# Optimization experiments

Hardware: AMD Instinct MI355X
Metric: run time of the kernel (lower is better)

## Reference

```python
import jax, jax.numpy as jnp
import numpy as np


def setup_inputs() -> dict:
    key = jax.random.key(0)
    x = jax.random.normal(key, (32, 512, 56, 56), dtype=jnp.float32)
    return {"x": x}


def reference(x):
    n, c, h, w = x.shape
    f = x.reshape(n, c, h * w)                       # (n, c, hw)
    f_norm = jax.nn.softmax(f * 7.0, axis=2)         # softmax over spatial
    bilinear = jnp.einsum('ncs,nds->ncd', f_norm, f) # (n, c, c)
    bilinear = jax.nn.softmax(bilinear, axis=2)      # softmax over channel 'keys'
    trilinear = jnp.einsum('ncd,nds->ncs', bilinear, f).reshape(n, c, h, w)
    trilinear = jax.lax.stop_gradient(trilinear)     # matches torch .detach()
    structure_att = jnp.sum(trilinear, axis=1, keepdims=True)  # (n, 1, h, w)
    return structure_att
```

## Files before the change

### kernel.cpp

```cpp
#include <hip/hip_runtime.h>
#include <stdint.h>


#define NB 32
#define CC 512
#define SS 3136
#define SCALE 7.0f

typedef float f32x4 __attribute__((ext_vector_type(4)));
typedef _Float16 f16x8 __attribute__((ext_vector_type(8)));
typedef _Float16 f16x4 __attribute__((ext_vector_type(4)));
typedef _Float16 f16x2 __attribute__((ext_vector_type(2)));

__device__ inline unsigned short f2bf(float f) {
  unsigned int u = __float_as_uint(f);
  u += 0x7fffu + ((u >> 16) & 1u);
  return (unsigned short)(u >> 16);
}
__device__ inline float bf2f(unsigned short u) {
  return __uint_as_float((uint32_t)u << 16);
}

__device__ inline float wredmax(float v) {
#pragma unroll
  for (int m = 32; m >= 1; m >>= 1) v = fmaxf(v, __shfl_xor(v, m, 64));
  return v;
}
__device__ inline float wredsum(float v) {
#pragma unroll
  for (int m = 32; m >= 1; m >>= 1) v += __shfl_xor(v, m, 64);
  return v;
}

__device__ inline void load_lds16(const void* g, void* l) {
  __builtin_amdgcn_global_load_lds(
      (const __attribute__((address_space(1))) void*)(uintptr_t)g,
      (__attribute__((address_space(3))) void*)(uintptr_t)l, 16, 0, 0);
}

__global__ __launch_bounds__(256) void k_prep(const float* __restrict__ x,
                                              unsigned short* __restrict__ t,
                                              float* __restrict__ inv7,
                                              float* __restrict__ mxv,
                                              float* __restrict__ esum) {
  const int row = blockIdx.x;
  const int tid = threadIdx.x;
  if (tid == 0) esum[row] = 0.f;
  const float4* xr = (const float4*)(x + (size_t)row * SS);
  float4 v0 = xr[tid];
  float4 v1 = xr[tid + 256];
  float4 v2 = xr[tid + 512];
  float4 v3 = (tid < 16) ? xr[768 + tid] : make_float4(-1e30f, -1e30f, -1e30f, -1e30f);

  float mx = fmaxf(fmaxf(fmaxf(v0.x, v0.y), fmaxf(v0.z, v0.w)),
             fmaxf(fmaxf(fmaxf(v1.x, v1.y), fmaxf(v1.z, v1.w)),
             fmaxf(fmaxf(fmaxf(v2.x, v2.y), fmaxf(v2.z, v2.w)),
                   fmaxf(fmaxf(v3.x, v3.y), fmaxf(v3.z, v3.w)))));
  __shared__ float redm[4], reds[4];
  mx = wredmax(mx);
  if ((tid & 63) == 0) redm[tid >> 6] = mx;
  __syncthreads();
  mx = fmaxf(fmaxf(redm[0], redm[1]), fmaxf(redm[2], redm[3]));

  float s = 0.f;
  f16x4 p0, p1, p2, p3;
#define TQ(dst, sv)                                        \
  {                                                        \
    _Float16 th = (_Float16)(SCALE * ((sv) - mx));         \
    (dst) = th;                                            \
    s += (float)(_Float16)__expf((float)th);               \
  }
  TQ(p0[0], v0.x) TQ(p0[1], v0.y) TQ(p0[2], v0.z) TQ(p0[3], v0.w)
  TQ(p1[0], v1.x) TQ(p1[1], v1.y) TQ(p1[2], v1.z) TQ(p1[3], v1.w)
  TQ(p2[0], v2.x) TQ(p2[1], v2.y) TQ(p2[2], v2.z) TQ(p2[3], v2.w)
  TQ(p3[0], v3.x) TQ(p3[1], v3.y) TQ(p3[2], v3.z) TQ(p3[3], v3.w)
#undef TQ
  s = wredsum(s);
  if ((tid & 63) == 0) reds[tid >> 6] = s;
  __syncthreads();

  f16x4* tr = (f16x4*)(t + (size_t)row * SS);
  tr[tid] = p0;
  tr[tid + 256] = p1;
  tr[tid + 512] = p2;
  if (tid < 16) tr[768 + tid] = p3;
  if (tid == 0) {
    const float stot = reds[0] + reds[1] + reds[2] + reds[3];
    inv7[row] = 1.0f / (SCALE * stot);
    mxv[row] = mx;
  }
}

#define BM 128
#define BK 64

__global__ __launch_bounds__(256) void k_gemm(const unsigned short* __restrict__ T,
                                              unsigned short* __restrict__ P,
                                              const float* __restrict__ inv7,
                                              const float* __restrict__ mxv,
                                              float* __restrict__ esum) {
  __shared__ unsigned short sA[BM * BK];
  __shared__ unsigned short sB[BM * BK];
  const int lin  = blockIdx.y * gridDim.x + blockIdx.x;
  const int xcd  = lin & 7;
  const int slot = lin >> 3;
  const int pair = xcd * 16 + (slot >> 2);
  const int n    = pair >> 2;
  const int tm   = (pair & 3) * BM;
  const int tn   = (slot & 3) * BM;
  const unsigned short* Ap = T + (size_t)n * CC * SS + (size_t)tm * SS;
  const unsigned short* Bp = T + (size_t)n * CC * SS + (size_t)tn * SS;
  const int tid  = threadIdx.x;
  const int lane = tid & 63;
  const int wave = tid >> 6;
  const int wm   = (wave >> 1) * 64;
  const int wn   = (wave & 1) * 64;
  const int quad = lane >> 4;
  const int rr   = lane & 15;

  f32x4 acc[4][4] = {};

  for (int k0 = 0; k0 < SS; k0 += BK) {
    f16x8 hv[4];
#pragma unroll
    for (int tt = 0; tt < 4; tt++) {
      const int j  = ((tt << 2) + wave) * 64 + lane;
      const int r  = j >> 3;
      const int cg = (j & 7) ^ (r & 7);
      hv[tt] = *(const f16x8*)(Ap + (size_t)r * SS + (k0 + cg * 8));
      load_lds16(Bp + (size_t)r * SS + (k0 + cg * 8), &sB[(size_t)j * 8]);
    }
#pragma unroll
    for (int tt = 0; tt < 4; tt++) {
      const int j = ((tt << 2) + wave) * 64 + lane;
      f16x8 ev;
#pragma unroll
      for (int u = 0; u < 8; u++) ev[u] = (_Float16)__expf((float)hv[tt][u]);
      *(f16x8*)&sA[(size_t)j * 8] = ev;
    }
    __syncthreads();
#pragma unroll
    for (int ki = 0; ki < 2; ki++) {
      f16x8 af[4], bfr[4];
      const int cg = ki * 4 + quad;
#pragma unroll
      for (int mt = 0; mt < 4; mt++) {
        const int r  = wm + mt * 16 + rr;
        const int cs = cg ^ (r & 7);
        af[mt] = *(const f16x8*)&sA[(r * 8 + cs) * 8];
      }
#pragma unroll
      for (int nt = 0; nt < 4; nt++) {
        const int r  = wn + nt * 16 + rr;
        const int cs = cg ^ (r & 7);
        bfr[nt] = *(const f16x8*)&sB[(r * 8 + cs) * 8];
      }
#pragma unroll
      for (int mt = 0; mt < 4; mt++)
#pragma unroll
        for (int nt = 0; nt < 4; nt++)
          acc[mt][nt] = __builtin_amdgcn_mfma_f32_16x16x32_f16(af[mt], bfr[nt], acc[mt][nt], 0, 0, 0);
    }
    __syncthreads();
  }

  unsigned short* Pp = P + ((size_t)n << 18);
  float mxd[4];
#pragma unroll
  for (int nt = 0; nt < 4; nt++) mxd[nt] = mxv[n * CC + tn + wn + nt * 16 + rr];
#pragma unroll
  for (int mt = 0; mt < 4; mt++) {
    const int rbase = tm + wm + mt * 16 + quad * 4;
    float iv[4];
#pragma unroll
    for (int i = 0; i < 4; i++) iv[i] = inv7[n * CC + rbase + i];
    float rs[4] = {0.f, 0.f, 0.f, 0.f};
#pragma unroll
    for (int nt = 0; nt < 4; nt++) {
      const int col = tn + wn + nt * 16 + rr;
#pragma unroll
      for (int i = 0; i < 4; i++) {
        const float e = __expf(acc[mt][nt][i] * iv[i] + mxd[nt]);
        rs[i] += e;
        Pp[(size_t)(rbase + i) * CC + col] = f2bf(e);
      }
    }
#pragma unroll
    for (int i = 0; i < 4; i++) {
      float v = rs[i];
#pragma unroll
      for (int m = 8; m >= 1; m >>= 1) v += __shfl_xor(v, m, 64);
      if (rr == 0) atomicAdd(&esum[n * CC + rbase + i], v);
    }
  }
}

__global__ __launch_bounds__(256) void k_wsum(const unsigned short* __restrict__ P,
                                              const float* __restrict__ esum,
                                              float* __restrict__ wp,
                                              float* __restrict__ outz) {
  const int lin  = blockIdx.y * gridDim.x + blockIdx.x;
  const int xcd  = lin & 7;
  const int slot = lin >> 3;
  const int n    = xcd * 4 + (slot & 3);
  const int g    = (slot >> 2) & 7;
  const int d    = (slot >> 5) * 256 + threadIdx.x;
  __shared__ float sinv[64];
  if (threadIdx.x < 64) sinv[threadIdx.x] = 1.0f / esum[n * CC + g * 64 + threadIdx.x];
  __syncthreads();
  const unsigned short* p = P + (size_t)n * CC * CC + (size_t)(g * 64) * CC + d;
  float acc = 0.f;
#pragma unroll 8
  for (int c = 0; c < 64; c++) acc += bf2f(p[(size_t)c * CC]) * sinv[c];
  wp[((size_t)n * 8 + g) * CC + d] = acc;
  const int idx = lin * 256 + threadIdx.x;
  if (idx < NB * SS) outz[idx] = 0.f;
}

__global__ __launch_bounds__(256) void k_out(const unsigned short* __restrict__ T,
                                             const float* __restrict__ wp,
                                             const float* __restrict__ mxv,
                                             float* __restrict__ out) {
  const int n  = blockIdx.y >> 2;
  const int dq = blockIdx.y & 3;
  const int s0 = (blockIdx.x * 256 + threadIdx.x) * 2;
  __shared__ float sw[128];
  __shared__ float sc[2];
  if (threadIdx.x < 128) {
    float v = 0.f;
#pragma unroll
    for (int g = 0; g < 8; g++) v += wp[((size_t)n * 8 + g) * CC + dq * 128 + threadIdx.x];
    sw[threadIdx.x] = v * (1.0f / SCALE);
    float pm = v * mxv[n * CC + dq * 128 + threadIdx.x];
    pm = wredsum(pm);
    if ((threadIdx.x & 63) == 0) sc[threadIdx.x >> 6] = pm;
  }
  __syncthreads();
  const float csum = sc[0] + sc[1];
  if (s0 >= SS) return;
  const unsigned short* bp = T + (size_t)n * CC * SS + (size_t)(dq * 128) * SS + s0;
  float a0 = 0.f, a1 = 0.f;
#pragma unroll 8
  for (int d = 0; d < 128; d++) {
    const f16x2 hv = *(const f16x2*)(bp + (size_t)d * SS);
    a0 += sw[d] * (float)hv[0];
    a1 += sw[d] * (float)hv[1];
  }
  atomicAdd(&out[(size_t)n * SS + s0], a0 + csum);
  atomicAdd(&out[(size_t)n * SS + s0 + 1], a1 + csum);
}

extern "C" void kernel_launch(void* const* d_in, const int* in_sizes, int n_in,
                              void* d_out, int out_size, void* d_ws, size_t ws_size,
                              hipStream_t stream) {
  const float* x = (const float*)d_in[0];
  float* out = (float*)d_out;
  char* ws = (char*)d_ws;
  unsigned short* t    = (unsigned short*)ws;
  unsigned short* pmat = (unsigned short*)(ws + 102760448ull);
  float* esum = (float*)(ws + 119537664ull);
  float* inv7 = (float*)(ws + 119603200ull);
  float* mxv  = (float*)(ws + 119668736ull);
  float* wp   = (float*)(ws + 119734272ull);

  hipLaunchKernelGGL(k_prep, dim3(NB * CC),   dim3(256), 0, stream, x, t, inv7, mxv, esum);
  hipLaunchKernelGGL(k_gemm, dim3(16, NB),    dim3(256), 0, stream, t, pmat, inv7, mxv, esum);
  hipLaunchKernelGGL(k_wsum, dim3(16, NB),    dim3(256), 0, stream, pmat, esum, wp, out);
  hipLaunchKernelGGL(k_out,  dim3(7, NB * 4), dim3(256), 0, stream, t, wp, mxv, out);
}
```

Baseline: 165.4 us.

## Double-buffer GEMM LDS tiles and use native exp2 with log2e-folded scale

The GEMM main loop now uses two LDS buffers, so the next tile's global loads are issued before the MFMA work on the current tile and exponentiated afterwards, letting load latency overlap with compute. The precompute stage now stores the scaled value in base-2 units (scale multiplied by log2 e), so the exponent in the GEMM becomes a single v_exp_f32 with packed f16 conversion instead of __expf. Later stages are rescaled to match. LDS use doubles to 64 KB per block with a two-block occupancy hint, which could limit occupancy or raise register pressure.

```diff
diff --git a/kernel.cpp b/kernel.cpp
--- a/kernel.cpp
+++ b/kernel.cpp
@@ -6,6 +6,8 @@
 #define CC 512
 #define SS 3136
 #define SCALE 7.0f
+#define K7F 10.098865286222744f
+#define INVK7F 0.09902102579427789f
 
 typedef float f32x4 __attribute__((ext_vector_type(4)));
 typedef _Float16 f16x8 __attribute__((ext_vector_type(8)));
@@ -19,6 +21,27 @@
 }
 __device__ inline float bf2f(unsigned short u) {
   return __uint_as_float((uint32_t)u << 16);
+}
+
+__device__ inline float fast_exp2(float v) {
+  float r;
+  asm("v_exp_f32 %0, %1" : "=v"(r) : "v"(v));
+  return r;
+}
+__device__ inline uint32_t pk2h(float a, float b) {
+  uint32_t r;
+  asm("v_cvt_pkrtz_f16_f32 %0, %1, %2" : "=v"(r) : "v"(a), "v"(b));
+  return r;
+}
+__device__ inline f16x8 exp2_f16x8(f16x8 h) {
+  f16x8 r;
+#pragma unroll
+  for (int q = 0; q < 4; q++) {
+    const float e0 = fast_exp2((float)h[2 * q]);
+    const float e1 = fast_exp2((float)h[2 * q + 1]);
+    ((uint32_t*)&r)[q] = pk2h(e0, e1);
+  }
+  return r;
 }
 
 __device__ inline float wredmax(float v) {
@@ -64,17 +87,20 @@
 
   float s = 0.f;
   f16x4 p0, p1, p2, p3;
-#define TQ(dst, sv)                                        \
-  {                                                        \
-    _Float16 th = (_Float16)(SCALE * ((sv) - mx));         \
-    (dst) = th;                                            \
-    s += (float)(_Float16)__expf((float)th);               \
-  }
-  TQ(p0[0], v0.x) TQ(p0[1], v0.y) TQ(p0[2], v0.z) TQ(p0[3], v0.w)
-  TQ(p1[0], v1.x) TQ(p1[1], v1.y) TQ(p1[2], v1.z) TQ(p1[3], v1.w)
-  TQ(p2[0], v2.x) TQ(p2[1], v2.y) TQ(p2[2], v2.z) TQ(p2[3], v2.w)
-  TQ(p3[0], v3.x) TQ(p3[1], v3.y) TQ(p3[2], v3.z) TQ(p3[3], v3.w)
-#undef TQ
+#define TQ2(dst, i0, a0, a1)                                  \
+  {                                                           \
+    _Float16 h0 = (_Float16)(K7F * ((a0) - mx));              \
+    _Float16 h1 = (_Float16)(K7F * ((a1) - mx));              \
+    dst[i0] = h0; dst[i0 + 1] = h1;                           \
+    uint32_t u = pk2h(fast_exp2((float)h0), fast_exp2((float)h1)); \
+    f16x2 e2; *(uint32_t*)&e2 = u;                            \
+    s += (float)e2[0] + (float)e2[1];                         \
+  }
+  TQ2(p0, 0, v0.x, v0.y) TQ2(p0, 2, v0.z, v0.w)
+  TQ2(p1, 0, v1.x, v1.y) TQ2(p1, 2, v1.z, v1.w)
+  TQ2(p2, 0, v2.x, v2.y) TQ2(p2, 2, v2.z, v2.w)
+  TQ2(p3, 0, v3.x, v3.y) TQ2(p3, 2, v3.z, v3.w)
+#undef TQ2
   s = wredsum(s);
   if ((tid & 63) == 0) reds[tid >> 6] = s;
   __syncthreads();
@@ -86,21 +112,22 @@
   if (tid < 16) tr[768 + tid] = p3;
   if (tid == 0) {
     const float stot = reds[0] + reds[1] + reds[2] + reds[3];
-    inv7[row] = 1.0f / (SCALE * stot);
+    inv7[row] = 1.0f / (K7F * stot);
     mxv[row] = mx;
   }
 }
 
 #define BM 128
 #define BK 64
-
-__global__ __launch_bounds__(256) void k_gemm(const unsigned short* __restrict__ T,
-                                              unsigned short* __restrict__ P,
-                                              const float* __restrict__ inv7,
-                                              const float* __restrict__ mxv,
-                                              float* __restrict__ esum) {
-  __shared__ unsigned short sA[BM * BK];
-  __shared__ unsigned short sB[BM * BK];
+#define NT (SS / BK)
+
+__global__ __launch_bounds__(256, 2) void k_gemm(const unsigned short* __restrict__ T,
+                                                 unsigned short* __restrict__ P,
+                                                 const float* __restrict__ inv7,
+                                                 const float* __restrict__ mxv,
+                                                 float* __restrict__ esum) {
+  __shared__ unsigned short sA[2][BM * BK];
+  __shared__ unsigned short sB[2][BM * BK];
   const int lin  = blockIdx.y * gridDim.x + blockIdx.x;
   const int xcd  = lin & 7;
   const int slot = lin >> 3;
@@ -118,51 +145,76 @@
   const int quad = lane >> 4;
   const int rr   = lane & 15;
 
+  int jb[4];
+  const unsigned short *Aaddr[4], *Baddr[4];
+#pragma unroll
+  for (int tt = 0; tt < 4; tt++) {
+    const int j  = ((tt << 2) + wave) * 64 + lane;
+    const int r  = j >> 3;
+    const int cg = (j & 7) ^ (r & 7);
+    jb[tt]   = j * 8;
+    Aaddr[tt] = Ap + (size_t)r * SS + cg * 8;
+    Baddr[tt] = Bp + (size_t)r * SS + cg * 8;
+  }
+
   f32x4 acc[4][4] = {};
 
-  for (int k0 = 0; k0 < SS; k0 += BK) {
+#define COMPUTE(BUF)                                                          \
+  {                                                                           \
+    _Pragma("unroll")                                                         \
+    for (int ki = 0; ki < 2; ki++) {                                          \
+      f16x8 af[4], bfr[4];                                                    \
+      const int cg = ki * 4 + quad;                                           \
+      _Pragma("unroll")                                                       \
+      for (int mt = 0; mt < 4; mt++) {                                        \
+        const int r  = wm + mt * 16 + rr;                                     \
+        const int cs = cg ^ (r & 7);                                          \
+        af[mt] = *(const f16x8*)&sA[BUF][(r * 8 + cs) * 8];                   \
+      }                                                                       \
+      _Pragma("unroll")                                                       \
+      for (int nt = 0; nt < 4; nt++) {                                        \
+        const int r  = wn + nt * 16 + rr;                                     \
+        const int cs = cg ^ (r & 7);                                          \
+        bfr[nt] = *(const f16x8*)&sB[BUF][(r * 8 + cs) * 8];                  \
+      }                                                                       \
+      _Pragma("unroll")                                                       \
+      for (int mt = 0; mt < 4; mt++)                                          \
+        _Pragma("unroll")                                                     \
+        for (int nt = 0; nt < 4; nt++)                                        \
+          acc[mt][nt] = __builtin_amdgcn_mfma_f32_16x16x32_f16(               \
+              af[mt], bfr[nt], acc[mt][nt], 0, 0, 0);                         \
+    }                                                                         \
+  }
+
+  {
     f16x8 hv[4];
 #pragma unroll
-    for (int tt = 0; tt < 4; tt++) {
-      const int j  = ((tt << 2) + wave) * 64 + lane;
-      const int r  = j >> 3;
-      const int cg = (j & 7) ^ (r & 7);
-      hv[tt] = *(const f16x8*)(Ap + (size_t)r * SS + (k0 + cg * 8));
-      load_lds16(Bp + (size_t)r * SS + (k0 + cg * 8), &sB[(size_t)j * 8]);
-    }
-#pragma unroll
-    for (int tt = 0; tt < 4; tt++) {
-      const int j = ((tt << 2) + wave) * 64 + lane;
-      f16x8 ev;
-#pragma unroll
-      for (int u = 0; u < 8; u++) ev[u] = (_Float16)__expf((float)hv[tt][u]);
-      *(f16x8*)&sA[(size_t)j * 8] = ev;
-    }
+    for (int tt = 0; tt < 4; tt++) hv[tt] = *(const f16x8*)Aaddr[tt];
+#pragma unroll
+    for (int tt = 0; tt < 4; tt++) load_lds16(Baddr[tt], &sB[0][jb[tt]]);
+#pragma unroll
+    for (int tt = 0; tt < 4; tt++) *(f16x8*)&sA[0][jb[tt]] = exp2_f16x8(hv[tt]);
     __syncthreads();
-#pragma unroll
-    for (int ki = 0; ki < 2; ki++) {
-      f16x8 af[4], bfr[4];
-      const int cg = ki * 4 + quad;
-#pragma unroll
-      for (int mt = 0; mt < 4; mt++) {
-        const int r  = wm + mt * 16 + rr;
-        const int cs = cg ^ (r & 7);
-        af[mt] = *(const f16x8*)&sA[(r * 8 + cs) * 8];
-      }
-#pragma unroll
-      for (int nt = 0; nt < 4; nt++) {
-        const int r  = wn + nt * 16 + rr;
-        const int cs = cg ^ (r & 7);
-        bfr[nt] = *(const f16x8*)&sB[(r * 8 + cs) * 8];
-      }
-#pragma unroll
-      for (int mt = 0; mt < 4; mt++)
-#pragma unroll
-        for (int nt = 0; nt < 4; nt++)
-          acc[mt][nt] = __builtin_amdgcn_mfma_f32_16x16x32_f16(af[mt], bfr[nt], acc[mt][nt], 0, 0, 0);
-    }
+  }
+
+  int cur = 0;
+  for (int t = 0; t < NT - 1; t++) {
+    const int koff = (t + 1) * BK;
+    const int nxt  = cur ^ 1;
+    f16x8 hvN[4];
+#pragma unroll
+    for (int tt = 0; tt < 4; tt++) hvN[tt] = *(const f16x8*)(Aaddr[tt] + koff);
+#pragma unroll
+    for (int tt = 0; tt < 4; tt++) load_lds16(Baddr[tt] + koff, &sB[nxt][jb[tt]]);
+
+    COMPUTE(cur);
+
+#pragma unroll
+    for (int tt = 0; tt < 4; tt++) *(f16x8*)&sA[nxt][jb[tt]] = exp2_f16x8(hvN[tt]);
     __syncthreads();
-  }
+    cur = nxt;
+  }
+  COMPUTE(cur);
 
   unsigned short* Pp = P + ((size_t)n << 18);
   float mxd[4];
@@ -193,6 +245,7 @@
       if (rr == 0) atomicAdd(&esum[n * CC + rbase + i], v);
     }
   }
+#undef COMPUTE
 }
 
 __global__ __launch_bounds__(256) void k_wsum(const unsigned short* __restrict__ P,
@@ -230,7 +283,7 @@
     float v = 0.f;
 #pragma unroll
     for (int g = 0; g < 8; g++) v += wp[((size_t)n * 8 + g) * CC + dq * 128 + threadIdx.x];
-    sw[threadIdx.x] = v * (1.0f / SCALE);
+    sw[threadIdx.x] = v * INVK7F;
     float pm = v * mxv[n * CC + dq * 128 + threadIdx.x];
     pm = wredsum(pm);
     if ((threadIdx.x & 63) == 0) sc[threadIdx.x >> 6] = pm;
```

After: 145.9 us, median of 2. 1.13x faster.
